# Kernel tuning notes

Hardware: AMD Instinct MI355X
Metric: run time of the kernel (lower is better)

Reference implementation:

```python
import jax, jax.numpy as jnp
import numpy as np

BANK_FILTERS = 64
DIM = 128
KSIZE = 3
BATCH = 256


def setup_inputs() -> dict:
    key = jax.random.key(0)
    k1, k2 = jax.random.split(key)
    bank_request = jax.random.normal(k1, (BATCH, BANK_FILTERS), dtype=jnp.float32)
    weight = jax.random.normal(k2, (BANK_FILTERS, DIM, DIM, KSIZE, KSIZE), dtype=jnp.float32)
    return {"bank_request": bank_request, "weight": weight}


def reference(bank_request, weight):
    # softmax over filter bank, then weighted sum of filters -> per-sample kernel
    probs = jax.nn.softmax(bank_request, axis=1)          # (B, F)
    Fb, D1, D2, K1, K2 = weight.shape
    # express as a single GEMM over the filter axis instead of broadcast-mul-reduce
    w2d = weight.reshape(Fb, D1 * D2 * K1 * K2)           # (F, D*D*k*k)
    kernel = probs @ w2d                                   # (B, D*D*k*k)
    return kernel.reshape(bank_request.shape[0], D1, D2, K1, K2)
```

## Files before the change

kernel.cpp:

```cpp
#include <hip/hip_runtime.h>
#include <math.h>

#define BATCH 256
#define FB    64
#define NCOL  147456
#define TPB   256
#define BT    32

#define FMA4(a, s, w) do { \
    (a).x = fmaf((s), (w).x, (a).x); \
    (a).y = fmaf((s), (w).y, (a).y); \
    (a).z = fmaf((s), (w).z, (a).z); \
    (a).w = fmaf((s), (w).w, (a).w); \
} while (0)

__global__ __launch_bounds__(TPB, 2) void bank_gemm_fused(
        const float* __restrict__ W, const float* __restrict__ X,
        float* __restrict__ out) {
    __shared__ float pt[FB * BT];

    const int tid = threadIdx.x;
    const int bg  = blockIdx.y;
    const int ncol4 = NCOL / 4;
    const float4* Wv = (const float4*)W;
    const int c4 = blockIdx.x * TPB + tid;

    float4 w = Wv[c4];

    const int wave = tid >> 6;
    const int lane = tid & 63;
#pragma unroll
    for (int r0 = 0; r0 < BT / 4; ++r0) {
        const int r = r0 * 4 + wave;
        float v = X[(bg * BT + r) * FB + lane];
        float m = v;
#pragma unroll
        for (int o = 32; o > 0; o >>= 1) m = fmaxf(m, __shfl_xor(m, o));
        float e = __expf(v - m);
        float s = e;
#pragma unroll
        for (int o = 32; o > 0; o >>= 1) s += __shfl_xor(s, o);
        pt[lane * BT + r] = e / s;
    }
    __syncthreads();

    float4 acc[BT];
#pragma unroll
    for (int b = 0; b < BT; ++b) acc[b] = make_float4(0.f, 0.f, 0.f, 0.f);

    for (int f = 0; f < FB; ++f) {
        float4 wn = w;
        if (f + 1 < FB) wn = Wv[(f + 1) * ncol4 + c4];
        const float4* p4 = (const float4*)&pt[f * BT];
#pragma unroll
        for (int q = 0; q < BT / 4; ++q) {
            const float4 p = p4[q];
            FMA4(acc[4 * q + 0], p.x, w);
            FMA4(acc[4 * q + 1], p.y, w);
            FMA4(acc[4 * q + 2], p.z, w);
            FMA4(acc[4 * q + 3], p.w, w);
        }
        w = wn;
    }

    float4* Ov = (float4*)out;
    const long long obase = (long long)(bg * BT) * ncol4 + c4;
#pragma unroll
    for (int b = 0; b < BT; ++b) {
        Ov[obase + (long long)b * ncol4] = acc[b];
    }
}

extern "C" void kernel_launch(void* const* d_in, const int* in_sizes, int n_in,
                              void* d_out, int out_size, void* d_ws, size_t ws_size,
                              hipStream_t stream) {
    const float* bank   = (const float*)d_in[0];
    const float* weight = (const float*)d_in[1];
    float* out   = (float*)d_out;
    (void)d_ws; (void)ws_size;

    dim3 grid(NCOL / (TPB * 4), BATCH / BT);
    bank_gemm_fused<<<grid, TPB, 0, stream>>>(weight, bank, out);
}
```

Before: 219.9 us.

## Halve batch tile, deepen weight prefetch, swizzle blocks across XCDs

Shrinks the batch tile from 32 to 16 rows per block, which halves the accumulator registers and raises the occupancy hint from 2 to 4 blocks per SM. The weight loads now run four filters ahead in a rotating register set instead of one. Block indices are remapped so each XCD handles a contiguous range of columns for all batch groups, aiming for better L2 reuse of weight tiles. The shared probability array is padded against bank conflicts. In exchange, the weight matrix is read twice as many times overall because there are twice as many batch groups, and the output offset now uses 32-bit arithmetic.

```diff
diff --git a/kernel.cpp b/kernel.cpp
--- a/kernel.cpp
+++ b/kernel.cpp
@@ -4,28 +4,40 @@
 #define BATCH 256
 #define FB    64
 #define NCOL  147456
+#define NCOL4 (NCOL / 4)
 #define TPB   256
-#define BT    32
+#define BT    16
+#define NBG   (BATCH / BT)
+#define NXB   (NCOL / (TPB * 4))
+#define PTS   (BT + 4)
 
-#define FMA4(a, s, w) do { \
-    (a).x = fmaf((s), (w).x, (a).x); \
-    (a).y = fmaf((s), (w).y, (a).y); \
-    (a).z = fmaf((s), (w).z, (a).z); \
-    (a).w = fmaf((s), (w).w, (a).w); \
+#define FMA4(A, S, WV) do { \
+    (A).x = fmaf((S), (WV).x, (A).x); \
+    (A).y = fmaf((S), (WV).y, (A).y); \
+    (A).z = fmaf((S), (WV).z, (A).z); \
+    (A).w = fmaf((S), (WV).w, (A).w); \
 } while (0)
 
-__global__ __launch_bounds__(TPB, 2) void bank_gemm_fused(
+__global__ __launch_bounds__(TPB, 4) void bank_gemm_fused(
         const float* __restrict__ W, const float* __restrict__ X,
         float* __restrict__ out) {
-    __shared__ float pt[FB * BT];
+    __shared__ float pt[FB * PTS];
 
     const int tid = threadIdx.x;
-    const int bg  = blockIdx.y;
-    const int ncol4 = NCOL / 4;
+
+    const int wg   = blockIdx.y * gridDim.x + blockIdx.x;
+    const int xcd  = wg & 7;
+    const int slot = wg >> 3;
+    const int bx   = xcd * (NXB / 8) + (slot >> 4);
+    const int bg   = slot & 15;
+
     const float4* Wv = (const float4*)W;
-    const int c4 = blockIdx.x * TPB + tid;
+    const int c4 = bx * TPB + tid;
 
-    float4 w = Wv[c4];
+    float4 wr0 = Wv[0 * NCOL4 + c4];
+    float4 wr1 = Wv[1 * NCOL4 + c4];
+    float4 wr2 = Wv[2 * NCOL4 + c4];
+    float4 wr3 = Wv[3 * NCOL4 + c4];
 
     const int wave = tid >> 6;
     const int lane = tid & 63;
@@ -40,7 +52,7 @@
         float s = e;
 #pragma unroll
         for (int o = 32; o > 0; o >>= 1) s += __shfl_xor(s, o);
-        pt[lane * BT + r] = e / s;
+        pt[lane * PTS + r] = e / s;
     }
     __syncthreads();
 
@@ -48,26 +60,54 @@
 #pragma unroll
     for (int b = 0; b < BT; ++b) acc[b] = make_float4(0.f, 0.f, 0.f, 0.f);
 
-    for (int f = 0; f < FB; ++f) {
-        float4 wn = w;
-        if (f + 1 < FB) wn = Wv[(f + 1) * ncol4 + c4];
-        const float4* p4 = (const float4*)&pt[f * BT];
-#pragma unroll
-        for (int q = 0; q < BT / 4; ++q) {
-            const float4 p = p4[q];
-            FMA4(acc[4 * q + 0], p.x, w);
-            FMA4(acc[4 * q + 1], p.y, w);
-            FMA4(acc[4 * q + 2], p.z, w);
-            FMA4(acc[4 * q + 3], p.w, w);
-        }
-        w = wn;
+#define STEP(J, WREG) do { \
+        const float4 wcur = (WREG); \
+        (WREG) = Wv[(f + 4 + (J)) * NCOL4 + c4]; \
+        const float4* p4 = (const float4*)&pt[(f + (J)) * PTS]; \
+        _Pragma("unroll") \
+        for (int q = 0; q < BT / 4; ++q) { \
+            const float4 p = p4[q];    \
+            FMA4(acc[4 * q + 0], p.x, wcur); \
+            FMA4(acc[4 * q + 1], p.y, wcur); \
+            FMA4(acc[4 * q + 2], p.z, wcur); \
+            FMA4(acc[4 * q + 3], p.w, wcur); \
+        } \
+    } while (0)
+
+#define TAIL(J, WREG) do { \
+        const float4 wcur = (WREG); \
+        const float4* p4 = (const float4*)&pt[(f + (J)) * PTS]; \
+        _Pragma("unroll") \
+        for (int q = 0; q < BT / 4; ++q) { \
+            const float4 p = p4[q]; \
+            FMA4(acc[4 * q + 0], p.x, wcur); \
+            FMA4(acc[4 * q + 1], p.y, wcur); \
+            FMA4(acc[4 * q + 2], p.z, wcur); \
+            FMA4(acc[4 * q + 3], p.w, wcur); \
+        } \
+    } while (0)
+
+    for (int f = 0; f < FB - 4; f += 4) {
+        STEP(0, wr0);
+        STEP(1, wr1);
+        STEP(2, wr2);
+        STEP(3, wr3);
     }
+    {
+        const int f = FB - 4;
+        TAIL(0, wr0);
+        TAIL(1, wr1);
+        TAIL(2, wr2);
+        TAIL(3, wr3);
+    }
+#undef STEP
+#undef TAIL
 
     float4* Ov = (float4*)out;
-    const long long obase = (long long)(bg * BT) * ncol4 + c4;
+    const int obase = (bg * BT) * NCOL4 + c4;
 #pragma unroll
     for (int b = 0; b < BT; ++b) {
-        Ov[obase + (long long)b * ncol4] = acc[b];
+        Ov[obase + b * NCOL4] = acc[b];
     }
 }
 
@@ -79,6 +119,6 @@
     float* out   = (float*)d_out;
     (void)d_ws; (void)ws_size;
 
-    dim3 grid(NCOL / (TPB * 4), BATCH / BT);
+    dim3 grid(NXB, NBG);
     bank_gemm_fused<<<grid, TPB, 0, stream>>>(weight, bank, out);
 }
```

Result: slower. 246.0 us (+11.9%).
